# Optimization experiments

Measured on AMD Instinct MI355X. Metric: run time of the kernel, lower is better.

## Reference

```python
import jax, jax.numpy as jnp
import numpy as np


def setup_inputs() -> dict:
    key = jax.random.key(0)
    k1, k2, k3, k4 = jax.random.split(key, 4)
    H = 256
    std = 1.0 / np.sqrt(H)
    x = jax.random.normal(k1, (64, 512, 128), dtype=jnp.float32)
    Wi = jax.random.uniform(k2, (128, 4 * H), dtype=jnp.float32, minval=-std, maxval=std)
    Wh = jax.random.uniform(k3, (H, 4 * H), dtype=jnp.float32, minval=-std, maxval=std)
    B = jax.random.uniform(k4, (4 * H,), dtype=jnp.float32, minval=-std, maxval=std)
    return {"x": x, "Wi": Wi, "Wh": Wh, "B": B}


def reference(x, Wi, Wh, B):
    bs, seqs, _ = x.shape
    H = Wh.shape[0]
    h0 = jnp.zeros((bs, H), dtype=x.dtype)
    c0 = jnp.zeros((bs, H), dtype=x.dtype)
    # Precompute input projections for all timesteps: [bs, seqs, 4H]
    xproj = jnp.einsum('bsi,ig->bsg', x, Wi) + B

    def step(carry, xp_t):
        ht, ct = carry
        gates = xp_t + ht @ Wh  # [bs, 4H]
        it = jax.nn.sigmoid(gates[:, :H])
        ft = jax.nn.sigmoid(gates[:, H:2 * H])
        gt = jnp.tanh(gates[:, 2 * H:3 * H])
        ot = jax.nn.sigmoid(gates[:, 3 * H:])
        ct = ft * ct + it * gt
        ht = ot * jnp.tanh(ct)
        return (ht, ct), ht

    (ht, ct), hs = jax.lax.scan(step, (h0, c0), jnp.swapaxes(xproj, 0, 1))
    output = jnp.swapaxes(hs, 0, 1)  # [bs, seqs, H]
    return (output, (ht, ct))
```

## Files before the change

### kernel.cpp

```cpp
#include <hip/hip_runtime.h>

#define BATCH 64
#define SEQ   512
#define INPD  128
#define HID   256
#define G4    1024
#define HSL   36


template<int CTRL>
__device__ __forceinline__ float dppf(float v) {
    return __int_as_float(__builtin_amdgcn_update_dpp(
        0, __float_as_int(v), CTRL, 0xF, 0xF, true));
}
#define DPP_XOR1 0xB1
#define DPP_XOR2 0x4E
#define DPP_HMIR 0x141

#define HROW(h, r) { \
    a0 = fmaf(h, wh[(r)*4+0], a0); a1 = fmaf(h, wh[(r)*4+1], a1); \
    a2 = fmaf(h, wh[(r)*4+2], a2); a3 = fmaf(h, wh[(r)*4+3], a3); }

#define XROW(h, r) { \
    a0 = fmaf(h, wi[(r)*4+0], a0); a1 = fmaf(h, wi[(r)*4+1], a1); \
    a2 = fmaf(h, wi[(r)*4+2], a2); a3 = fmaf(h, wi[(r)*4+3], a3); }

#define XPART_ALL { \
    a0 = nx0.x * wi[0]; a1 = nx0.x * wi[1]; a2 = nx0.x * wi[2]; a3 = nx0.x * wi[3]; \
    XROW(nx0.y, 1)  XROW(nx0.z, 2)  XROW(nx0.w, 3) \
    XROW(nx1.x, 4)  XROW(nx1.y, 5)  XROW(nx1.z, 6)  XROW(nx1.w, 7) \
    XROW(nx2.x, 8)  XROW(nx2.y, 9)  XROW(nx2.z, 10) XROW(nx2.w, 11) \
    XROW(nx3.x, 12) XROW(nx3.y, 13) XROW(nx3.z, 14) XROW(nx3.w, 15) }

__global__ __launch_bounds__(512, 2)
void ChaoticLSTM_kernel(const float* __restrict__ x,  const float* __restrict__ Wi,
                        const float* __restrict__ Wh, const float* __restrict__ Bb,
                        float* __restrict__ out, unsigned long long* __restrict__ exch)
{
    const int bid   = blockIdx.x;
    const int xcd   = bid & 7;
    const int slotn = bid >> 3;
    const int b     = xcd * 8 + (slotn >> 2);
    const int part  = slotn & 3;
    const int tid   = threadIdx.x;
    const int CG    = tid >> 3;
    const int S     = tid & 7;

    __shared__ __align__(16) float hbuf[2][8 * HSL];

    float wh[128];
    float wi[64];
    {
        const int col = part * 64 + CG;
#pragma unroll
        for (int r = 0; r < 32; ++r) {
            const float* p = Wh + (size_t)(S * 32 + r) * G4 + col;
            wh[r*4+0] = p[0]; wh[r*4+1] = p[256]; wh[r*4+2] = p[512]; wh[r*4+3] = p[768];
        }
#pragma unroll
        for (int r = 0; r < 16; ++r) {
            const float* p = Wi + (size_t)(S * 16 + r) * G4 + col;
            wi[r*4+0] = p[0]; wi[r*4+1] = p[256]; wi[r*4+2] = p[512]; wi[r*4+3] = p[768];
        }
    }
    const float bb0 = Bb[part*64 + CG],       bb1 = Bb[256 + part*64 + CG];
    const float bb2 = Bb[512 + part*64 + CG], bb3 = Bb[768 + part*64 + CG];

    unsigned long long* __restrict__ exb = exch + (size_t)b * 512;
    const float* __restrict__ xrow = x + (size_t)b * SEQ * INPD + S * 16;

    const bool is_own  = (S == 1);
    const int  jglob   = part * 64 + CG;
    const bool is_poll = (S >= 2 && S <= 4);
    int pidx = 0;
    if (is_poll) {
        int p = CG * 3 + (S - 2);
        pidx = (((part + 1 + (p >> 6)) & 3) << 6) + (p & 63);
    }

    float cs = 0.f, hn_keep = 0.f;
    if (tid < 256) hbuf[0][(tid >> 5) * HSL + (tid & 31)] = 0.f;
    if (tid < 64) {
        __hip_atomic_store(&exb[part*64 + tid],       0ull, __ATOMIC_RELAXED, __HIP_MEMORY_SCOPE_AGENT);
        __hip_atomic_store(&exb[256 + part*64 + tid], 0ull, __ATOMIC_RELAXED, __HIP_MEMORY_SCOPE_AGENT);
    }

    float a0, a1, a2, a3;
    {
        float4 nx0 = *(const float4*)(xrow);
        float4 nx1 = *(const float4*)(xrow + 4);
        float4 nx2 = *(const float4*)(xrow + 8);
        float4 nx3 = *(const float4*)(xrow + 12);
        XPART_ALL;
    }
    __syncthreads();

    for (int st = 0; st < SEQ; ++st) {
        const float* xp = xrow + (size_t)((st + 1 < SEQ) ? st + 1 : st) * INPD;
        float4 nx0 = *(const float4*)(xp);
        float4 nx1 = *(const float4*)(xp + 4);
        float4 nx2 = *(const float4*)(xp + 8);
        float4 nx3 = *(const float4*)(xp + 12);

        {
            const float* hb = hbuf[st & 1] + S * HSL;
            float4 hv;
            hv = *(const float4*)(hb);      HROW(hv.x, 0)  HROW(hv.y, 1)  HROW(hv.z, 2)  HROW(hv.w, 3)
            hv = *(const float4*)(hb + 4);  HROW(hv.x, 4)  HROW(hv.y, 5)  HROW(hv.z, 6)  HROW(hv.w, 7)
            hv = *(const float4*)(hb + 8);  HROW(hv.x, 8)  HROW(hv.y, 9)  HROW(hv.z, 10) HROW(hv.w, 11)
            hv = *(const float4*)(hb + 12); HROW(hv.x, 12) HROW(hv.y, 13) HROW(hv.z, 14) HROW(hv.w, 15)
            hv = *(const float4*)(hb + 16); HROW(hv.x, 16) HROW(hv.y, 17) HROW(hv.z, 18) HROW(hv.w, 19)
            hv = *(const float4*)(hb + 20); HROW(hv.x, 20) HROW(hv.y, 21) HROW(hv.z, 22) HROW(hv.w, 23)
            hv = *(const float4*)(hb + 24); HROW(hv.x, 24) HROW(hv.y, 25) HROW(hv.z, 26) HROW(hv.w, 27)
            hv = *(const float4*)(hb + 28); HROW(hv.x, 28) HROW(hv.y, 29) HROW(hv.z, 30) HROW(hv.w, 31)
        }

        a0 += dppf<DPP_XOR1>(a0); a1 += dppf<DPP_XOR1>(a1); a2 += dppf<DPP_XOR1>(a2); a3 += dppf<DPP_XOR1>(a3);
        a0 += dppf<DPP_XOR2>(a0); a1 += dppf<DPP_XOR2>(a1); a2 += dppf<DPP_XOR2>(a2); a3 += dppf<DPP_XOR2>(a3);
        a0 += dppf<DPP_HMIR>(a0); a1 += dppf<DPP_HMIR>(a1); a2 += dppf<DPP_HMIR>(a2); a3 += dppf<DPP_HMIR>(a3);
        a0 += bb0; a1 += bb1; a2 += bb2; a3 += bb3;

        const int r = S & 3;
        float xs = (r & 1) ? ((r & 2) ? a3 : a1) : ((r & 2) ? a2 : a0);
        float kk = (r == 2) ? 2.f : 1.f;
        float e  = __expf(-kk * xs);
        float z  = __builtin_amdgcn_rcpf(1.f + e);
        z = fmaf(z, kk, 1.f - kk);
        float zg = dppf<DPP_XOR2>(z);
        float p  = z * zg;
        float pp = dppf<DPP_XOR1>(p);
        float cn = fmaf(z, cs, pp);
        float e2 = __expf(-2.f * cn);
        float tc = fmaf(__builtin_amdgcn_rcpf(1.f + e2), 2.f, -1.f);
        float hn = tc * zg;
        cs = cn;

        const unsigned tag = (unsigned)(st + 1);
        unsigned long long* slotp = exb + (st & 1) * 256;
        float* hbn = hbuf[(st + 1) & 1];
        if (is_own) {
            hn_keep = hn;
            unsigned long long w = ((unsigned long long)tag << 32)
                                 | (unsigned long long)__float_as_uint(hn);
            if (st + 1 < SEQ)
                __hip_atomic_store(&slotp[jglob], w, __ATOMIC_RELAXED, __HIP_MEMORY_SCOPE_AGENT);
            hbn[(jglob >> 5) * HSL + (jglob & 31)] = hn;
            out[(size_t)(b * SEQ + st) * HID + jglob] = hn;
        }
        unsigned long long v = 0;
        const bool pl = is_poll && (st + 1 < SEQ);
        if (pl) v = __hip_atomic_load(&slotp[pidx], __ATOMIC_RELAXED, __HIP_MEMORY_SCOPE_AGENT);
        if (st + 1 < SEQ) { XPART_ALL }
        if (pl) {
            while ((unsigned)(v >> 32) != tag)
                v = __hip_atomic_load(&slotp[pidx], __ATOMIC_RELAXED, __HIP_MEMORY_SCOPE_AGENT);
            hbn[(pidx >> 5) * HSL + (pidx & 31)] = __uint_as_float((unsigned)v);
        }
        __syncthreads();
    }

    if (is_own) {
        size_t base = (size_t)BATCH * SEQ * HID;
        out[base + (size_t)b * HID + jglob] = hn_keep;
        out[base + (size_t)BATCH * HID + (size_t)b * HID + jglob] = cs;
    }
}

extern "C" void kernel_launch(void* const* d_in, const int* in_sizes, int n_in,
                              void* d_out, int out_size, void* d_ws, size_t ws_size,
                              hipStream_t stream) {
    const float* x  = (const float*)d_in[0];
    const float* Wi = (const float*)d_in[1];
    const float* Wh = (const float*)d_in[2];
    const float* B  = (const float*)d_in[3];
    float* out = (float*)d_out;
    unsigned long long* exch = (unsigned long long*)d_ws;

    ChaoticLSTM_kernel<<<dim3(256), dim3(512), 0, stream>>>(x, Wi, Wh, B, out, exch);
}
```

Baseline: 885.5 us.

## Overlap remote hidden-state polling with partial matvec via per-part LDS flags

```diff
diff --git a/kernel.cpp b/kernel.cpp
--- a/kernel.cpp
+++ b/kernel.cpp
@@ -5,7 +5,6 @@
 #define INPD  128
 #define HID   256
 #define G4    1024
-#define HSL   36
 
 
 template<int CTRL>
@@ -17,20 +16,24 @@
 #define DPP_XOR2 0x4E
 #define DPP_HMIR 0x141
 
-#define HROW(h, r) { \
-    a0 = fmaf(h, wh[(r)*4+0], a0); a1 = fmaf(h, wh[(r)*4+1], a1); \
-    a2 = fmaf(h, wh[(r)*4+2], a2); a3 = fmaf(h, wh[(r)*4+3], a3); }
+#define HROW4(base, h) { \
+    a0 = fmaf(h, wh[(base)+0], a0); a1 = fmaf(h, wh[(base)+1], a1); \
+    a2 = fmaf(h, wh[(base)+2], a2); a3 = fmaf(h, wh[(base)+3], a3); }
 
-#define XROW(h, r) { \
+#define HCHUNK(q, h0, h1) { \
+    HROW4((q)*32+ 0, h0.x) HROW4((q)*32+ 4, h0.y) HROW4((q)*32+ 8, h0.z) HROW4((q)*32+12, h0.w) \
+    HROW4((q)*32+16, h1.x) HROW4((q)*32+20, h1.y) HROW4((q)*32+24, h1.z) HROW4((q)*32+28, h1.w) }
+
+#define XROW(r, h) { \
     a0 = fmaf(h, wi[(r)*4+0], a0); a1 = fmaf(h, wi[(r)*4+1], a1); \
     a2 = fmaf(h, wi[(r)*4+2], a2); a3 = fmaf(h, wi[(r)*4+3], a3); }
 
 #define XPART_ALL { \
-    a0 = nx0.x * wi[0]; a1 = nx0.x * wi[1]; a2 = nx0.x * wi[2]; a3 = nx0.x * wi[3]; \
-    XROW(nx0.y, 1)  XROW(nx0.z, 2)  XROW(nx0.w, 3) \
-    XROW(nx1.x, 4)  XROW(nx1.y, 5)  XROW(nx1.z, 6)  XROW(nx1.w, 7) \
-    XROW(nx2.x, 8)  XROW(nx2.y, 9)  XROW(nx2.z, 10) XROW(nx2.w, 11) \
-    XROW(nx3.x, 12) XROW(nx3.y, 13) XROW(nx3.z, 14) XROW(nx3.w, 15) }
+    a0 = nx0.x*wi[0]; a1 = nx0.x*wi[1]; a2 = nx0.x*wi[2]; a3 = nx0.x*wi[3]; \
+    XROW(1, nx0.y)  XROW(2, nx0.z)  XROW(3, nx0.w) \
+    XROW(4, nx1.x)  XROW(5, nx1.y)  XROW(6, nx1.z)  XROW(7, nx1.w) \
+    XROW(8, nx2.x)  XROW(9, nx2.y)  XROW(10, nx2.z) XROW(11, nx2.w) \
+    XROW(12, nx3.x) XROW(13, nx3.y) XROW(14, nx3.z) XROW(15, nx3.w) }
 
 __global__ __launch_bounds__(512, 2)
 void ChaoticLSTM_kernel(const float* __restrict__ x,  const float* __restrict__ Wi,
@@ -45,74 +48,97 @@
     const int tid   = threadIdx.x;
     const int CG    = tid >> 3;
     const int S     = tid & 7;
+    const int jglob = part * 64 + CG;
+    const int wav   = tid >> 6;
 
-    __shared__ __align__(16) float hbuf[2][8 * HSL];
+    __shared__ __align__(16) float hp[4][2][64];
+    __shared__ int flg[4][2];
 
     float wh[128];
     float wi[64];
-    {
-        const int col = part * 64 + CG;
 #pragma unroll
-        for (int r = 0; r < 32; ++r) {
-            const float* p = Wh + (size_t)(S * 32 + r) * G4 + col;
-            wh[r*4+0] = p[0]; wh[r*4+1] = p[256]; wh[r*4+2] = p[512]; wh[r*4+3] = p[768];
-        }
+    for (int q = 0; q < 4; ++q) {
+        const int psrc = (part + q) & 3;
 #pragma unroll
-        for (int r = 0; r < 16; ++r) {
-            const float* p = Wi + (size_t)(S * 16 + r) * G4 + col;
-            wi[r*4+0] = p[0]; wi[r*4+1] = p[256]; wi[r*4+2] = p[512]; wi[r*4+3] = p[768];
+        for (int r = 0; r < 8; ++r) {
+            const float* p = Wh + (size_t)(psrc * 64 + S * 8 + r) * G4 + jglob;
+            wh[q*32 + r*4 + 0] = p[0];   wh[q*32 + r*4 + 1] = p[256];
+            wh[q*32 + r*4 + 2] = p[512]; wh[q*32 + r*4 + 3] = p[768];
         }
     }
-    const float bb0 = Bb[part*64 + CG],       bb1 = Bb[256 + part*64 + CG];
-    const float bb2 = Bb[512 + part*64 + CG], bb3 = Bb[768 + part*64 + CG];
+#pragma unroll
+    for (int r = 0; r < 16; ++r) {
+        const float* p = Wi + (size_t)(S * 16 + r) * G4 + jglob;
+        wi[r*4+0] = p[0]; wi[r*4+1] = p[256]; wi[r*4+2] = p[512]; wi[r*4+3] = p[768];
+    }
+    const float bb0 = Bb[jglob],       bb1 = Bb[256 + jglob];
+    const float bb2 = Bb[512 + jglob], bb3 = Bb[768 + jglob];
 
     unsigned long long* __restrict__ exb = exch + (size_t)b * 512;
     const float* __restrict__ xrow = x + (size_t)b * SEQ * INPD + S * 16;
 
-    const bool is_own  = (S == 1);
-    const int  jglob   = part * 64 + CG;
-    const bool is_poll = (S >= 2 && S <= 4);
-    int pidx = 0;
-    if (is_poll) {
-        int p = CG * 3 + (S - 2);
-        pidx = (((part + 1 + (p >> 6)) & 3) << 6) + (p & 63);
-    }
+    const bool is_own = (S == 1);
+    const bool is_pw  = (wav >= 5);
+    const int  pq     = is_pw ? (8 - wav) : 0;
+    const int  ppart  = (part + pq) & 3;
+    const int  plane  = tid & 63;
 
-    float cs = 0.f, hn_keep = 0.f;
-    if (tid < 256) hbuf[0][(tid >> 5) * HSL + (tid & 31)] = 0.f;
+    if (tid < 512) ((float*)hp)[tid] = 0.f;
+    if (tid < 8) ((int*)flg)[tid] = 0;
     if (tid < 64) {
         __hip_atomic_store(&exb[part*64 + tid],       0ull, __ATOMIC_RELAXED, __HIP_MEMORY_SCOPE_AGENT);
         __hip_atomic_store(&exb[256 + part*64 + tid], 0ull, __ATOMIC_RELAXED, __HIP_MEMORY_SCOPE_AGENT);
     }
+    float cs = 0.f, hn_keep = 0.f;
 
-    float a0, a1, a2, a3;
-    {
-        float4 nx0 = *(const float4*)(xrow);
-        float4 nx1 = *(const float4*)(xrow + 4);
-        float4 nx2 = *(const float4*)(xrow + 8);
-        float4 nx3 = *(const float4*)(xrow + 12);
-        XPART_ALL;
-    }
+    float4 nx0 = *(const float4*)(xrow);
+    float4 nx1 = *(const float4*)(xrow + 4);
+    float4 nx2 = *(const float4*)(xrow + 8);
+    float4 nx3 = *(const float4*)(xrow + 12);
     __syncthreads();
 
     for (int st = 0; st < SEQ; ++st) {
-        const float* xp = xrow + (size_t)((st + 1 < SEQ) ? st + 1 : st) * INPD;
-        float4 nx0 = *(const float4*)(xp);
-        float4 nx1 = *(const float4*)(xp + 4);
-        float4 nx2 = *(const float4*)(xp + 8);
-        float4 nx3 = *(const float4*)(xp + 12);
+        const int par = st & 1;
+
+        if (is_pw && st >= 1) {
+            unsigned long long* sp = exb + par * 256 + ppart * 64;
+            unsigned long long v =
+                __hip_atomic_load(&sp[plane], __ATOMIC_RELAXED, __HIP_MEMORY_SCOPE_AGENT);
+            while ((unsigned)(v >> 32) != (unsigned)st)
+                v = __hip_atomic_load(&sp[plane], __ATOMIC_RELAXED, __HIP_MEMORY_SCOPE_AGENT);
+            hp[ppart][par][plane] = __uint_as_float((unsigned)v);
+            if (plane == 0)
+                __hip_atomic_store(&flg[ppart][par], st, __ATOMIC_RELEASE, __HIP_MEMORY_SCOPE_WORKGROUP);
+        }
+
+        float a0, a1, a2, a3;
+        XPART_ALL;
+        {
+            const float4* hb = (const float4*)&hp[part][par][S * 8];
+            float4 h0 = hb[0], h1 = hb[1];
+            HCHUNK(0, h0, h1)
+        }
 
         {
-            const float* hb = hbuf[st & 1] + S * HSL;
-            float4 hv;
-            hv = *(const float4*)(hb);      HROW(hv.x, 0)  HROW(hv.y, 1)  HROW(hv.z, 2)  HROW(hv.w, 3)
-            hv = *(const float4*)(hb + 4);  HROW(hv.x, 4)  HROW(hv.y, 5)  HROW(hv.z, 6)  HROW(hv.w, 7)
-            hv = *(const float4*)(hb + 8);  HROW(hv.x, 8)  HROW(hv.y, 9)  HROW(hv.z, 10) HROW(hv.w, 11)
-            hv = *(const float4*)(hb + 12); HROW(hv.x, 12) HROW(hv.y, 13) HROW(hv.z, 14) HROW(hv.w, 15)
-            hv = *(const float4*)(hb + 16); HROW(hv.x, 16) HROW(hv.y, 17) HROW(hv.z, 18) HROW(hv.w, 19)
-            hv = *(const float4*)(hb + 20); HROW(hv.x, 20) HROW(hv.y, 21) HROW(hv.z, 22) HROW(hv.w, 23)
-            hv = *(const float4*)(hb + 24); HROW(hv.x, 24) HROW(hv.y, 25) HROW(hv.z, 26) HROW(hv.w, 27)
-            hv = *(const float4*)(hb + 28); HROW(hv.x, 28) HROW(hv.y, 29) HROW(hv.z, 30) HROW(hv.w, 31)
+            const float* xp = xrow + (size_t)((st + 1 < SEQ) ? st + 1 : st) * INPD;
+            nx0 = *(const float4*)(xp);
+            nx1 = *(const float4*)(xp + 4);
+            nx2 = *(const float4*)(xp + 8);
+            nx3 = *(const float4*)(xp + 12);
+        }
+
+#pragma unroll
+        for (int q = 1; q < 4; ++q) {
+            const int psrc = (part + q) & 3;
+            if (st >= 1) {
+                while (__hip_atomic_load(&flg[psrc][par], __ATOMIC_ACQUIRE,
+                                         __HIP_MEMORY_SCOPE_WORKGROUP) != st) {}
+            }
+            const float4* hb = (const float4*)&hp[psrc][par][S * 8];
+            float4 h0 = hb[0], h1 = hb[1];
+            if (q == 1) { HCHUNK(1, h0, h1) }
+            else if (q == 2) { HCHUNK(2, h0, h1) }
+            else { HCHUNK(3, h0, h1) }
         }
 
         a0 += dppf<DPP_XOR1>(a0); a1 += dppf<DPP_XOR1>(a1); a2 += dppf<DPP_XOR1>(a2); a3 += dppf<DPP_XOR1>(a3);
@@ -135,26 +161,16 @@
         float hn = tc * zg;
         cs = cn;
 
-        const unsigned tag = (unsigned)(st + 1);
-        unsigned long long* slotp = exb + (st & 1) * 256;
-        float* hbn = hbuf[(st + 1) & 1];
         if (is_own) {
             hn_keep = hn;
-            unsigned long long w = ((unsigned long long)tag << 32)
-                                 | (unsigned long long)__float_as_uint(hn);
-            if (st + 1 < SEQ)
-                __hip_atomic_store(&slotp[jglob], w, __ATOMIC_RELAXED, __HIP_MEMORY_SCOPE_AGENT);
-            hbn[(jglob >> 5) * HSL + (jglob & 31)] = hn;
+            if (st + 1 < SEQ) {
+                unsigned long long w = ((unsigned long long)(st + 1) << 32)
+                                     | (unsigned long long)__float_as_uint(hn);
+                __hip_atomic_store(&exb[((st + 1) & 1) * 256 + jglob], w,
+                                   __ATOMIC_RELAXED, __HIP_MEMORY_SCOPE_AGENT);
+            }
+            hp[part][(st + 1) & 1][CG] = hn;
             out[(size_t)(b * SEQ + st) * HID + jglob] = hn;
-        }
-        unsigned long long v = 0;
-        const bool pl = is_poll && (st + 1 < SEQ);
-        if (pl) v = __hip_atomic_load(&slotp[pidx], __ATOMIC_RELAXED, __HIP_MEMORY_SCOPE_AGENT);
-        if (st + 1 < SEQ) { XPART_ALL }
-        if (pl) {
-            while ((unsigned)(v >> 32) != tag)
-                v = __hip_atomic_load(&slotp[pidx], __ATOMIC_RELAXED, __HIP_MEMORY_SCOPE_AGENT);
-            hbn[(pidx >> 5) * HSL + (pidx & 31)] = __uint_as_float((unsigned)v);
         }
         __syncthreads();
     }
```

After: 1.395 ms. 1.58x slower.
